# Kernel optimization log

Measured on AMD Instinct MI355X. Metric: run time of the kernel, lower is better.

The kernel has to match this reference:

```python
import jax, jax.numpy as jnp
import numpy as np

N_QUBITS = 11
N_CIRCUITS = 3
N_ROTS = 6
BATCH = 512
C64 = jnp.complex64


def _ry_mat(theta):
    # RY(t) = [[cos t/2, -sin t/2], [sin t/2, cos t/2]]
    c = jnp.cos(theta * 0.5)
    s = jnp.sin(theta * 0.5)
    return jnp.stack([jnp.stack([c, -s]), jnp.stack([s, c])]).astype(C64)


def _rz_mat(theta):
    # RZ(t) = diag(e^{-i t/2}, e^{+i t/2})
    e = jnp.exp((-0.5j) * theta.astype(C64))
    z = jnp.zeros_like(e)
    return jnp.stack([jnp.stack([e, z]), jnp.stack([z, jnp.conj(e)])])


def _apply_1q(state, U, q):
    # state: (2,)*n complex; apply 2x2 U on axis q (PennyLane wire q = axis q)
    out = jnp.tensordot(U, state, axes=((1,), (q,)))
    return jnp.moveaxis(out, 0, q)


def _apply_ctrl(state, U, c, t):
    # controlled-U on wires [c(control), t(target)]: block_diag(I2, U) in |c t> basis
    U4 = jnp.eye(4, dtype=C64).at[2:, 2:].set(U)
    out = jnp.tensordot(U4.reshape(2, 2, 2, 2), state, axes=((2, 3), (c, t)))
    return jnp.moveaxis(out, (0, 1), (c, t))


def _simulate(angles):
    # angles: [n_circuits, 6, n_qubits] -> expvals [2*n_qubits] (X then Z)
    n = N_QUBITS
    state = jnp.zeros((2,) * n, dtype=C64).at[(0,) * n].set(1.0)
    for i in range(N_CIRCUITS):
        for q in range(n):
            state = _apply_1q(state, _ry_mat(angles[i, 0, q]), q)
            state = _apply_1q(state, _rz_mat(angles[i, 1, q]), q)
            state = _apply_1q(state, _ry_mat(angles[i, 2, q]), q)
            state = _apply_1q(state, _rz_mat(angles[i, 3, q]), q)
        for q in range(n):
            t = (q + 1) % n
            state = _apply_ctrl(state, _ry_mat(angles[i, 4, q]), q, t)
            state = _apply_ctrl(state, _rz_mat(angles[i, 5, q]), q, t)
    ex_x, ex_z = [], []
    for q in range(n):
        s0 = jnp.take(state, 0, axis=q)
        s1 = jnp.take(state, 1, axis=q)
        # <X_q> = 2 Re <psi_{q=0}|psi_{q=1}>,  <Z_q> = p(q=0) - p(q=1)
        ex_x.append(2.0 * jnp.real(jnp.vdot(s0, s1)))
        ex_z.append(jnp.sum(jnp.abs(s0) ** 2 - jnp.abs(s1) ** 2))
    return jnp.stack(ex_x + ex_z).astype(jnp.float32)


def setup_inputs() -> dict:
    key = jax.random.key(0)
    k1, k2, k3 = jax.random.split(key, 3)
    x = jax.random.normal(k1, (BATCH, N_QUBITS), dtype=jnp.float32)
    W = jax.random.uniform(k2, (N_CIRCUITS, N_QUBITS * N_ROTS, N_QUBITS),
                           dtype=jnp.float32, minval=-0.01, maxval=0.01)
    b = jax.random.uniform(k3, (N_CIRCUITS, N_QUBITS * N_ROTS),
                           dtype=jnp.float32, minval=-0.01, maxval=0.01)
    return {"x": x, "W": W, "b": b}


def reference(x, W, b):
    # per-circuit Linear (dropout is identity in eval): [B, C, n_rots*n_qubits]
    rot = jnp.einsum('coi,bi->bco', W, x) + b[None, :, :]
    angles = rot.reshape(x.shape[0], N_CIRCUITS, N_ROTS, N_QUBITS)
    return jax.vmap(_simulate)(angles)  # [B, 2*n_qubits]
```

## Files before the change

### kernel.cpp

```cpp
#include <hip/hip_runtime.h>

#define NQ 11
#define NC 3
#define NANG (NC * 66)
#define BLOCK 512

typedef float f2 __attribute__((ext_vector_type(2)));

__device__ __forceinline__ f2 swp(f2 v) { return __builtin_shufflevector(v, v, 1, 0); }

template<int CTRL>
__device__ __forceinline__ float dppx(float v) {
  return __int_as_float(__builtin_amdgcn_update_dpp(
      0, __float_as_int(v), CTRL, 0xF, 0xF, false));
}
template<int CTRL>
__device__ __forceinline__ f2 dpp2(f2 v) {
  f2 r; r.x = dppx<CTRL>(v.x); r.y = dppx<CTRL>(v.y); return r;
}
template<int OFF>
__device__ __forceinline__ float swz1(float v) {
  return __int_as_float(__builtin_amdgcn_ds_swizzle(__float_as_int(v), OFF));
}
template<int OFF>
__device__ __forceinline__ f2 swz2(f2 v) {
  f2 r; r.x = swz1<OFF>(v.x); r.y = swz1<OFF>(v.y); return r;
}
__device__ __forceinline__ float plp16(float v, int lane) {
  auto r = __builtin_amdgcn_permlane16_swap(__float_as_int(v), __float_as_int(v), false, false);
  return __int_as_float((lane & 16) ? r[0] : r[1]);
}
__device__ __forceinline__ float plp32(float v, int lane) {
  auto r = __builtin_amdgcn_permlane32_swap(__float_as_int(v), __float_as_int(v), false, false);
  return __int_as_float((lane & 32) ? r[0] : r[1]);
}
__device__ __forceinline__ f2 plp16_2(f2 v, int lane) {
  f2 r; r.x = plp16(v.x, lane); r.y = plp16(v.y, lane); return r;
}
__device__ __forceinline__ f2 plp32_2(f2 v, int lane) {
  f2 r; r.x = plp32(v.x, lane); r.y = plp32(v.y, lane); return r;
}
__device__ __forceinline__ float plsum16(float v) {
  auto r = __builtin_amdgcn_permlane16_swap(__float_as_int(v), __float_as_int(v), false, false);
  return __int_as_float(r[0]) + __int_as_float(r[1]);
}
__device__ __forceinline__ float plsum32(float v) {
  auto r = __builtin_amdgcn_permlane32_swap(__float_as_int(v), __float_as_int(v), false, false);
  return __int_as_float(r[0]) + __int_as_float(r[1]);
}

__device__ __forceinline__ void apply2p(f2& v0, f2& v1, float4 U) {
  const f2 ai2 = {-U.y, U.y};
  const f2 bi2 = {-U.w, U.w};
  const f2 w0 = swp(v0), w1 = swp(v1);
  const f2 n0 =  U.x * v0 + ai2 * w0 + U.z * v1 + bi2 * w1;
  const f2 n1 = -U.z * v0 + bi2 * w0 + U.x * v1 - ai2 * w1;
  v0 = n0; v1 = n1;
}
__device__ __forceinline__ void gpartp(f2& v, f2 p, float4 U, bool hi) {
  const f2 ai2 = hi ? f2{U.y, -U.y} : f2{-U.y, U.y};
  const float br = hi ? -U.z : U.z;
  const f2 bi2 = {-U.w, U.w};
  v = U.x * v + ai2 * swp(v) + br * p + bi2 * swp(p);
}

__device__ __forceinline__ f2 cmul(f2 u, f2 v) {
  return f2{u.x * v.x - u.y * v.y, u.x * v.y + u.y * v.x};
}
__device__ __forceinline__ void rowof(float4 G, bool hi, f2& c0, f2& c1) {
  c0 = hi ? f2{-G.z, G.w} : f2{G.x, G.y};
  c1 = hi ? f2{G.x, -G.y} : f2{G.z, G.w};
}

__device__ __forceinline__ void g_wave3(f2 (&s)[4], float4 A, float4 B, float4 C,
                                        f2* __restrict__ buf, int wave, int lane) {
  const int base = (wave << 6) | lane;
#pragma unroll
  for (int i = 0; i < 4; ++i) buf[(i << 9) | base] = s[i];
  f2 a0, a1, b0, b1, c0, c1;
  rowof(A, (wave & 4) != 0, a0, a1);
  rowof(B, (wave & 2) != 0, b0, b1);
  rowof(C, (wave & 1) != 0, c0, c1);
  const f2 d00 = cmul(b0, c0), d01 = cmul(b0, c1);
  const f2 d10 = cmul(b1, c0), d11 = cmul(b1, c1);
  f2 r[8];
  r[0] = cmul(a0, d00); r[1] = cmul(a0, d01); r[2] = cmul(a0, d10); r[3] = cmul(a0, d11);
  r[4] = cmul(a1, d00); r[5] = cmul(a1, d01); r[6] = cmul(a1, d10); r[7] = cmul(a1, d11);
  __syncthreads();
#pragma unroll
  for (int i = 0; i < 4; ++i) {
    f2 acc = {0.f, 0.f};
#pragma unroll
    for (int w2 = 0; w2 < 8; ++w2) {
      const f2 p = buf[(i << 9) | (w2 << 6) | lane];
      acc += r[w2].x * p + f2{-r[w2].y, r[w2].y} * swp(p);
    }
    s[i] = acc;
  }
}

__global__ __launch_bounds__(BLOCK) void qsim_kernel(
    const float* __restrict__ x, const float* __restrict__ W,
    const float* __restrict__ bias, float* __restrict__ out) {
  const int bidx = blockIdx.x;
  const int tid = threadIdx.x;
  const int lane = tid & 63, wave = tid >> 6;

  __shared__ float xs[NQ];
  __shared__ float ang[NANG];
  __shared__ float4 m1s[NC * NQ];
  __shared__ float4 m2s[NC * NQ];
  __shared__ float4 v1s[NC * 10];
  __shared__ f2 ex0[2048];
  __shared__ f2 ex1[2048];
  __shared__ float red[8][24];

  if (tid < NQ) xs[tid] = x[bidx * NQ + tid];
  __syncthreads();

  if (tid < NANG) {
    const int c = tid / 66, o = tid - c * 66;
    const float* wr = W + (c * 66 + o) * NQ;
    float s = bias[c * 66 + o];
#pragma unroll
    for (int i = 0; i < NQ; ++i) s += wr[i] * xs[i];
    ang[tid] = s;
  }
  __syncthreads();

  if (tid < 2 * NC * NQ) {
    const int kind = tid / (NC * NQ);
    const int id = tid - kind * (NC * NQ);
    const int c = id / NQ, q = id - c * NQ;
    const float* a = ang + c * 66;
    if (kind == 0) {
      float s0,c0,s1,c1,s2,c2,s3,c3;
      sincosf(0.5f*a[q],      &s0,&c0);
      sincosf(0.5f*a[11+q],   &s1,&c1);
      sincosf(0.5f*a[22+q],   &s2,&c2);
      sincosf(0.5f*a[33+q],   &s3,&c3);
      const float mar = c1*c0, mai = -s1*c0;
      const float mbr = -c1*s0, mbi = s1*s0;
      const float nar = c2*mar + s2*mbr, nai = c2*mai - s2*mbi;
      const float nbr = c2*mbr - s2*mar, nbi = c2*mbi + s2*mai;
      m1s[id] = make_float4(c3*nar + s3*nai, c3*nai - s3*nar,
                            c3*nbr + s3*nbi, c3*nbi - s3*nbr);
    } else {
      float s4,c4,s5,c5;
      sincosf(0.5f*a[44+q], &s4,&c4);
      sincosf(0.5f*a[55+q], &s5,&c5);
      m2s[id] = make_float4(c5*c4, -s5*c4, -c5*s4, s5*s4);
    }
  }
  __syncthreads();

  if (tid < NC * 10) {
    const int c = tid / 10, tt = tid - c * 10, t = tt + 1;
    const float4 A = m2s[c*NQ + t - 1];
    const float4 B = m1s[c*NQ + t];
    const float pr_=A.x, pi_=A.y, qr_=A.z, qi_=A.w;
    const float ar_=B.x, ai_=B.y, br_=B.z, bi_=B.w;
    v1s[c*10 + tt] = make_float4(
      (pr_*ar_ - pi_*ai_) - (qr_*br_ + qi_*bi_),
      (pr_*ai_ + pi_*ar_) - (qi_*br_ - qr_*bi_),
      (pr_*br_ - pi_*bi_) + (qr_*ar_ + qi_*ai_),
      (pr_*bi_ + pi_*br_) + (qi_*ar_ - qr_*ai_));
  }
  __syncthreads();

  f2 s[4];
#pragma unroll
  for (int i = 0; i < 4; ++i) s[i] = f2{0.f, 0.f};
  if (tid == 0) s[0].x = 1.f;

  for (int c = 0; c < NC; ++c) {
    const float4* M1 = &m1s[c * NQ];
    const float4* VF = &v1s[c * 10];
    {
      apply2p(s[0], s[1], M1[0]);
      apply2p(s[2], s[3], M1[0]);
    }
    g_pl32_regsel: ;
    {
      const bool hi = (lane & 32) != 0;
#pragma unroll
      for (int i = 0; i < 4; ++i)
        gpartp(s[i], plp32_2(s[i], lane), (i & 1) ? VF[0] : M1[1], hi);
    }
    {
      const float4 U = *((lane & 32) ? &VF[1] : &M1[2]);
      const bool hi = (lane & 16) != 0;
#pragma unroll
      for (int i = 0; i < 4; ++i) gpartp(s[i], plp16_2(s[i], lane), U, hi);
    }
    {
      const float4 U = *((lane & 16) ? &VF[2] : &M1[3]);
      const bool hi = (lane & 8) != 0;
#pragma unroll
      for (int i = 0; i < 4; ++i) gpartp(s[i], swz2<0x201F>(s[i]), U, hi);
    }
    {
      const float4 A = *((lane & 8) ? &VF[3] : &M1[4]);
      const float4 B = *((wave & 4) ? &VF[4] : &M1[5]);
      const float4 C = *((wave & 2) ? &VF[5] : &M1[6]);
      g_wave3(s, A, B, C, (c & 1) ? ex1 : ex0, wave, lane);
    }
    {
      const float4 U = *((wave & 1) ? &VF[6] : &M1[7]);
      const bool hi = (lane & 4) != 0;
#pragma unroll
      for (int i = 0; i < 4; ++i) gpartp(s[i], swz2<0x101F>(s[i]), U, hi);
    }
    {
      const float4 U = *((lane & 4) ? &VF[7] : &M1[8]);
      const bool hi = (lane & 2) != 0;
#pragma unroll
      for (int i = 0; i < 4; ++i) gpartp(s[i], dpp2<0x4E>(s[i]), U, hi);
    }
    {
      const float4 U = *((lane & 2) ? &VF[8] : &M1[9]);
      const bool hi = (lane & 1) != 0;
#pragma unroll
      for (int i = 0; i < 4; ++i) gpartp(s[i], dpp2<0xB1>(s[i]), U, hi);
    }
    {
      const float4 U = *((lane & 1) ? &VF[9] : &M1[10]);
      apply2p(s[0], s[2], U);
      apply2p(s[1], s[3], U);
    }
    {
      apply2p(s[2], s[3], m2s[c * NQ + 10]);
    }
  }

  f2* eb = ex1;
  const int base = (wave << 6) | lane;
#pragma unroll
  for (int i = 0; i < 4; ++i) eb[(i << 9) | base] = s[i];
  __syncthreads();
  const int pb4 = ((wave ^ 4) << 6) | lane;
  const int pb2 = ((wave ^ 2) << 6) | lane;
  const int pb1 = ((wave ^ 1) << 6) | lane;
  f2 aq4 = {0,0}, aq5 = {0,0}, aq6 = {0,0};
#pragma unroll
  for (int i = 0; i < 4; ++i) {
    aq4 += s[i] * eb[(i << 9) | pb4];
    aq5 += s[i] * eb[(i << 9) | pb2];
    aq6 += s[i] * eb[(i << 9) | pb1];
  }
  f2 mg[4];
#pragma unroll
  for (int i = 0; i < 4; ++i) mg[i] = s[i] * s[i];
  const f2 ztv  = (mg[0] + mg[1]) + (mg[2] + mg[3]);
  const f2 z0v  = (mg[0] - mg[1]) + (mg[2] - mg[3]);
  const f2 z10v = (mg[0] + mg[1]) - (mg[2] + mg[3]);
  f2 aq0={0,0}, aq10={0,0}, aq9={0,0}, aq8={0,0}, aq7={0,0}, aq3={0,0}, aq2={0,0}, aq1={0,0};
#pragma unroll
  for (int i = 0; i < 4; ++i) {
    aq0  += s[i] * s[i ^ 1];
    aq10 += s[i] * s[i ^ 2];
    aq9  += s[i] * dpp2<0xB1>(s[i]);
    aq8  += s[i] * dpp2<0x4E>(s[i]);
    aq7  += s[i] * swz2<0x101F>(s[i]);
    aq3  += s[i] * swz2<0x201F>(s[i]);
    aq2  += s[i] * plp16_2(s[i], lane);
    aq1  += s[i] * plp32_2(s[i], lane);
  }
  const float ztot = ztv.x + ztv.y;

  float v[22];
  v[0]=aq0.x+aq0.y; v[1]=aq1.x+aq1.y; v[2]=aq2.x+aq2.y; v[3]=aq3.x+aq3.y;
  v[4]=aq4.x+aq4.y; v[5]=aq5.x+aq5.y; v[6]=aq6.x+aq6.y;
  v[7]=aq7.x+aq7.y; v[8]=aq8.x+aq8.y; v[9]=aq9.x+aq9.y; v[10]=aq10.x+aq10.y;
  v[11] = z0v.x + z0v.y;
  v[12] = (lane & 32) ? -ztot : ztot;
  v[13] = (lane & 16) ? -ztot : ztot;
  v[14] = (lane & 8)  ? -ztot : ztot;
  v[15] = (wave & 4)  ? -ztot : ztot;
  v[16] = (wave & 2)  ? -ztot : ztot;
  v[17] = (wave & 1)  ? -ztot : ztot;
  v[18] = (lane & 4)  ? -ztot : ztot;
  v[19] = (lane & 2)  ? -ztot : ztot;
  v[20] = (lane & 1)  ? -ztot : ztot;
  v[21] = z10v.x + z10v.y;

#pragma unroll
  for (int k = 0; k < 22; ++k) {
    v[k] += dppx<0xB1>(v[k]);
    v[k] += dppx<0x4E>(v[k]);
  }
  const int q4l = lane & 3;
  float wv[6];
#pragma unroll
  for (int p = 0; p < 5; ++p)
    wv[p] = q4l == 0 ? v[4*p] : (q4l == 1 ? v[4*p+1] : (q4l == 2 ? v[4*p+2] : v[4*p+3]));
  wv[5] = q4l == 0 ? v[20] : (q4l == 1 ? v[21] : 0.f);
#pragma unroll
  for (int p = 0; p < 6; ++p) {
    wv[p] += swz1<0x101F>(wv[p]);
    wv[p] += swz1<0x201F>(wv[p]);
    wv[p] = plsum16(wv[p]);
    wv[p] = plsum32(wv[p]);
  }
  if (lane < 4) {
#pragma unroll
    for (int p = 0; p < 6; ++p) red[wave][4*p + lane] = wv[p];
  }
  __syncthreads();
  if (tid < 22) {
    float sacc = 0.f;
#pragma unroll
    for (int w8 = 0; w8 < 8; ++w8) sacc += red[w8][tid];
    out[bidx * 22 + tid] = sacc;
  }
}

extern "C" void kernel_launch(void* const* d_in, const int* in_sizes, int n_in,
                              void* d_out, int out_size, void* d_ws, size_t ws_size,
                              hipStream_t stream) {
  (void)n_in; (void)d_ws; (void)ws_size; (void)out_size;
  const float* x = (const float*)d_in[0];
  const float* W = (const float*)d_in[1];
  const float* b = (const float*)d_in[2];
  float* out = (float*)d_out;
  const int batch = in_sizes[0] / NQ;
  qsim_kernel<<<batch, BLOCK, 0, stream>>>(x, W, b, out);
}
```

Baseline: 23.76 us.

## Compute gate matrices per wave and split cross-wave gate into pairwise exchanges

Each wave now redundantly computes the angles, rotation matrices and fused gate products in its own shared-memory slice. This removes the block-wide barriers from the setup phase. The three-qubit cross-wave gate is replaced by three pairwise exchanges through double-buffered shared memory, each reading one partner value instead of eight. The last controlled gate of each layer is also fused with the next layer's first single-qubit gate. In exchange, the cross-wave step needs three barriers per layer instead of one, and every wave repeats the setup work, including loads of W.

New measurement: 24.52 us. +3.2%, slower.

```diff
diff --git a/kernel.cpp b/kernel.cpp
--- a/kernel.cpp
+++ b/kernel.cpp
@@ -2,7 +2,6 @@
 
 #define NQ 11
 #define NC 3
-#define NANG (NC * 66)
 #define BLOCK 512
 
 typedef float f2 __attribute__((ext_vector_type(2)));
@@ -63,40 +62,23 @@
   const f2 bi2 = {-U.w, U.w};
   v = U.x * v + ai2 * swp(v) + br * p + bi2 * swp(p);
 }
-
-__device__ __forceinline__ f2 cmul(f2 u, f2 v) {
-  return f2{u.x * v.x - u.y * v.y, u.x * v.y + u.y * v.x};
-}
-__device__ __forceinline__ void rowof(float4 G, bool hi, f2& c0, f2& c1) {
-  c0 = hi ? f2{-G.z, G.w} : f2{G.x, G.y};
-  c1 = hi ? f2{G.x, -G.y} : f2{G.z, G.w};
-}
-
-__device__ __forceinline__ void g_wave3(f2 (&s)[4], float4 A, float4 B, float4 C,
-                                        f2* __restrict__ buf, int wave, int lane) {
+__device__ __forceinline__ float4 su2mul(float4 A, float4 B) {
+  return make_float4(
+    (A.x*B.x - A.y*B.y) - (A.z*B.z + A.w*B.w),
+    (A.x*B.y + A.y*B.x) - (A.w*B.z - A.z*B.w),
+    (A.x*B.z - A.y*B.w) + (A.z*B.x + A.w*B.y),
+    (A.x*B.w + A.y*B.z) + (A.w*B.x - A.z*B.y));
+}
+template<int WVX>
+__device__ __forceinline__ void g_wave(f2 (&s)[4], float4 U, f2* buf, int wave, int lane) {
   const int base = (wave << 6) | lane;
 #pragma unroll
   for (int i = 0; i < 4; ++i) buf[(i << 9) | base] = s[i];
-  f2 a0, a1, b0, b1, c0, c1;
-  rowof(A, (wave & 4) != 0, a0, a1);
-  rowof(B, (wave & 2) != 0, b0, b1);
-  rowof(C, (wave & 1) != 0, c0, c1);
-  const f2 d00 = cmul(b0, c0), d01 = cmul(b0, c1);
-  const f2 d10 = cmul(b1, c0), d11 = cmul(b1, c1);
-  f2 r[8];
-  r[0] = cmul(a0, d00); r[1] = cmul(a0, d01); r[2] = cmul(a0, d10); r[3] = cmul(a0, d11);
-  r[4] = cmul(a1, d00); r[5] = cmul(a1, d01); r[6] = cmul(a1, d10); r[7] = cmul(a1, d11);
   __syncthreads();
-#pragma unroll
-  for (int i = 0; i < 4; ++i) {
-    f2 acc = {0.f, 0.f};
-#pragma unroll
-    for (int w2 = 0; w2 < 8; ++w2) {
-      const f2 p = buf[(i << 9) | (w2 << 6) | lane];
-      acc += r[w2].x * p + f2{-r[w2].y, r[w2].y} * swp(p);
-    }
-    s[i] = acc;
-  }
+  const int pbase = ((wave ^ WVX) << 6) | lane;
+  const bool hi = (wave & WVX) != 0;
+#pragma unroll
+  for (int i = 0; i < 4; ++i) gpartp(s[i], buf[(i << 9) | pbase], U, hi);
 }
 
 __global__ __launch_bounds__(BLOCK) void qsim_kernel(
@@ -106,81 +88,95 @@
   const int tid = threadIdx.x;
   const int lane = tid & 63, wave = tid >> 6;
 
-  __shared__ float xs[NQ];
-  __shared__ float ang[NANG];
-  __shared__ float4 m1s[NC * NQ];
-  __shared__ float4 m2s[NC * NQ];
-  __shared__ float4 v1s[NC * 10];
+  __shared__ float  angw[8 * 198];
+  __shared__ float4 m1w[8 * 33];
+  __shared__ float4 m2w[8 * 33];
+  __shared__ float4 vw[8 * 30];
+  __shared__ float4 jw[8 * 2];
   __shared__ f2 ex0[2048];
   __shared__ f2 ex1[2048];
   __shared__ float red[8][24];
 
-  if (tid < NQ) xs[tid] = x[bidx * NQ + tid];
-  __syncthreads();
-
-  if (tid < NANG) {
-    const int c = tid / 66, o = tid - c * 66;
-    const float* wr = W + (c * 66 + o) * NQ;
-    float s = bias[c * 66 + o];
-#pragma unroll
-    for (int i = 0; i < NQ; ++i) s += wr[i] * xs[i];
-    ang[tid] = s;
-  }
-  __syncthreads();
-
-  if (tid < 2 * NC * NQ) {
-    const int kind = tid / (NC * NQ);
-    const int id = tid - kind * (NC * NQ);
+  float xr[NQ];
+#pragma unroll
+  for (int i = 0; i < NQ; ++i) xr[i] = x[bidx * NQ + i];
+
+  float* aw = angw + wave * 198;
+#pragma unroll
+  for (int r3 = 0; r3 < 3; ++r3) {
+    const int id = lane + 64 * r3;
+    const float* wr = W + id * NQ;
+    float s = bias[id];
+#pragma unroll
+    for (int i = 0; i < NQ; ++i) s += wr[i] * xr[i];
+    aw[id] = s;
+  }
+  if (lane < 6) {
+    const int id = 192 + lane;
+    const float* wr = W + id * NQ;
+    float s = bias[id];
+#pragma unroll
+    for (int i = 0; i < NQ; ++i) s += wr[i] * xr[i];
+    aw[id] = s;
+  }
+
+  float4* M1W = m1w + wave * 33;
+  float4* M2W = m2w + wave * 33;
+  float4* VW  = vw + wave * 30;
+  float4* JW  = jw + wave * 2;
+  if (lane < 33) {
+    const int id = lane, c = id / NQ, q = id - c * NQ;
+    const float* a = aw + c * 66;
+    float s0,c0,s1,c1,s2,c2,s3,c3;
+    sincosf(0.5f*a[q],      &s0,&c0);
+    sincosf(0.5f*a[11+q],   &s1,&c1);
+    sincosf(0.5f*a[22+q],   &s2,&c2);
+    sincosf(0.5f*a[33+q],   &s3,&c3);
+    const float mar = c1*c0, mai = -s1*c0;
+    const float mbr = -c1*s0, mbi = s1*s0;
+    const float nar = c2*mar + s2*mbr, nai = c2*mai - s2*mbi;
+    const float nbr = c2*mbr - s2*mar, nbi = c2*mbi + s2*mai;
+    M1W[id] = make_float4(c3*nar + s3*nai, c3*nai - s3*nar,
+                          c3*nbr + s3*nbi, c3*nbi - s3*nbr);
+  } else {
+    const int id = lane - 33;
     const int c = id / NQ, q = id - c * NQ;
-    const float* a = ang + c * 66;
-    if (kind == 0) {
-      float s0,c0,s1,c1,s2,c2,s3,c3;
-      sincosf(0.5f*a[q],      &s0,&c0);
-      sincosf(0.5f*a[11+q],   &s1,&c1);
-      sincosf(0.5f*a[22+q],   &s2,&c2);
-      sincosf(0.5f*a[33+q],   &s3,&c3);
-      const float mar = c1*c0, mai = -s1*c0;
-      const float mbr = -c1*s0, mbi = s1*s0;
-      const float nar = c2*mar + s2*mbr, nai = c2*mai - s2*mbi;
-      const float nbr = c2*mbr - s2*mar, nbi = c2*mbi + s2*mai;
-      m1s[id] = make_float4(c3*nar + s3*nai, c3*nai - s3*nar,
-                            c3*nbr + s3*nbi, c3*nbi - s3*nbr);
-    } else {
-      float s4,c4,s5,c5;
-      sincosf(0.5f*a[44+q], &s4,&c4);
-      sincosf(0.5f*a[55+q], &s5,&c5);
-      m2s[id] = make_float4(c5*c4, -s5*c4, -c5*s4, s5*s4);
-    }
-  }
-  __syncthreads();
-
-  if (tid < NC * 10) {
-    const int c = tid / 10, tt = tid - c * 10, t = tt + 1;
-    const float4 A = m2s[c*NQ + t - 1];
-    const float4 B = m1s[c*NQ + t];
-    const float pr_=A.x, pi_=A.y, qr_=A.z, qi_=A.w;
-    const float ar_=B.x, ai_=B.y, br_=B.z, bi_=B.w;
-    v1s[c*10 + tt] = make_float4(
-      (pr_*ar_ - pi_*ai_) - (qr_*br_ + qi_*bi_),
-      (pr_*ai_ + pi_*ar_) - (qi_*br_ - qr_*bi_),
-      (pr_*br_ - pi_*bi_) + (qr_*ar_ + qi_*ai_),
-      (pr_*bi_ + pi_*br_) + (qi_*ar_ - qr_*ai_));
-  }
-  __syncthreads();
+    const float* a = aw + c * 66;
+    float s4,c4,s5,c5;
+    sincosf(0.5f*a[44+q], &s4,&c4);
+    sincosf(0.5f*a[55+q], &s5,&c5);
+    M2W[id] = make_float4(c5*c4, -s5*c4, -c5*s4, s5*s4);
+  }
+  if (lane < 2) {
+    const int id = 31 + lane;
+    const int c = id / NQ, q = id - c * NQ;
+    const float* a = aw + c * 66;
+    float s4,c4,s5,c5;
+    sincosf(0.5f*a[44+q], &s4,&c4);
+    sincosf(0.5f*a[55+q], &s5,&c5);
+    M2W[id] = make_float4(c5*c4, -s5*c4, -c5*s4, s5*s4);
+  }
+  if (lane < 30) {
+    const int c = lane / 10, tt = lane - c * 10, t = tt + 1;
+    VW[lane] = su2mul(M2W[c*NQ + t - 1], M1W[c*NQ + t]);
+  } else if (lane < 32) {
+    const int cc = lane - 30;
+    JW[cc] = su2mul(M1W[(cc + 1) * NQ], M2W[cc * NQ + 10]);
+  }
 
   f2 s[4];
 #pragma unroll
   for (int i = 0; i < 4; ++i) s[i] = f2{0.f, 0.f};
   if (tid == 0) s[0].x = 1.f;
 
+  int par = 0;
   for (int c = 0; c < NC; ++c) {
-    const float4* M1 = &m1s[c * NQ];
-    const float4* VF = &v1s[c * 10];
-    {
+    const float4* M1 = M1W + c * NQ;
+    const float4* VF = VW + c * 10;
+    if (c == 0) {
       apply2p(s[0], s[1], M1[0]);
       apply2p(s[2], s[3], M1[0]);
     }
-    g_pl32_regsel: ;
     {
       const bool hi = (lane & 32) != 0;
 #pragma unroll
@@ -199,12 +195,9 @@
 #pragma unroll
       for (int i = 0; i < 4; ++i) gpartp(s[i], swz2<0x201F>(s[i]), U, hi);
     }
-    {
-      const float4 A = *((lane & 8) ? &VF[3] : &M1[4]);
-      const float4 B = *((wave & 4) ? &VF[4] : &M1[5]);
-      const float4 C = *((wave & 2) ? &VF[5] : &M1[6]);
-      g_wave3(s, A, B, C, (c & 1) ? ex1 : ex0, wave, lane);
-    }
+    g_wave<4>(s, *((lane & 8) ? &VF[3] : &M1[4]), par ? ex1 : ex0, wave, lane); par ^= 1;
+    g_wave<2>(s, *((wave & 4) ? &VF[4] : &M1[5]), par ? ex1 : ex0, wave, lane); par ^= 1;
+    g_wave<1>(s, *((wave & 2) ? &VF[5] : &M1[6]), par ? ex1 : ex0, wave, lane); par ^= 1;
     {
       const float4 U = *((wave & 1) ? &VF[6] : &M1[7]);
       const bool hi = (lane & 4) != 0;
@@ -228,12 +221,15 @@
       apply2p(s[0], s[2], U);
       apply2p(s[1], s[3], U);
     }
-    {
-      apply2p(s[2], s[3], m2s[c * NQ + 10]);
-    }
-  }
-
-  f2* eb = ex1;
+    if (c < 2) {
+      apply2p(s[0], s[1], M1W[(c + 1) * NQ]);
+      apply2p(s[2], s[3], JW[c]);
+    } else {
+      apply2p(s[2], s[3], M2W[32]);
+    }
+  }
+
+  f2* eb = par ? ex1 : ex0;
   const int base = (wave << 6) | lane;
 #pragma unroll
   for (int i = 0; i < 4; ++i) eb[(i << 9) | base] = s[i];
```

## Remap state to 256 threads with 8 amplitudes each, pairwise cross-wave gates

Applied to the files above, without the earlier changes.

Halves the block to 256 threads, so each thread holds 8 amplitudes instead of 4 and the 2048-amplitude state is remapped across lanes, waves and registers. The single three-qubit cross-wave gate through LDS is replaced by two one-qubit exchanges through LDS. The first gate of the next circuit is fused with the last controlled gate of the current one via precomputed SU(2) products. The aim is less LDS traffic per exchange and fewer threads per circuit, at the cost of more registers per thread, an extra barrier per circuit, and a rewired expectation-value mapping.

New measurement: 20.26 us (median of 2 runs). -14.7%, faster.

```diff
diff --git a/kernel.cpp b/kernel.cpp
--- a/kernel.cpp
+++ b/kernel.cpp
@@ -3,7 +3,7 @@
 #define NQ 11
 #define NC 3
 #define NANG (NC * 66)
-#define BLOCK 512
+#define BLOCK 256
 
 typedef float f2 __attribute__((ext_vector_type(2)));
 
@@ -63,40 +63,23 @@
   const f2 bi2 = {-U.w, U.w};
   v = U.x * v + ai2 * swp(v) + br * p + bi2 * swp(p);
 }
-
-__device__ __forceinline__ f2 cmul(f2 u, f2 v) {
-  return f2{u.x * v.x - u.y * v.y, u.x * v.y + u.y * v.x};
-}
-__device__ __forceinline__ void rowof(float4 G, bool hi, f2& c0, f2& c1) {
-  c0 = hi ? f2{-G.z, G.w} : f2{G.x, G.y};
-  c1 = hi ? f2{G.x, -G.y} : f2{G.z, G.w};
-}
-
-__device__ __forceinline__ void g_wave3(f2 (&s)[4], float4 A, float4 B, float4 C,
-                                        f2* __restrict__ buf, int wave, int lane) {
+__device__ __forceinline__ float4 su2mul(float4 A, float4 B) {
+  return make_float4(
+    (A.x*B.x - A.y*B.y) - (A.z*B.z + A.w*B.w),
+    (A.x*B.y + A.y*B.x) - (A.w*B.z - A.z*B.w),
+    (A.x*B.z - A.y*B.w) + (A.z*B.x + A.w*B.y),
+    (A.x*B.w + A.y*B.z) + (A.w*B.x - A.z*B.y));
+}
+template<int WVX>
+__device__ __forceinline__ void g_wave8(f2 (&s)[8], float4 U, f2* buf, int wave, int lane) {
   const int base = (wave << 6) | lane;
 #pragma unroll
-  for (int i = 0; i < 4; ++i) buf[(i << 9) | base] = s[i];
-  f2 a0, a1, b0, b1, c0, c1;
-  rowof(A, (wave & 4) != 0, a0, a1);
-  rowof(B, (wave & 2) != 0, b0, b1);
-  rowof(C, (wave & 1) != 0, c0, c1);
-  const f2 d00 = cmul(b0, c0), d01 = cmul(b0, c1);
-  const f2 d10 = cmul(b1, c0), d11 = cmul(b1, c1);
-  f2 r[8];
-  r[0] = cmul(a0, d00); r[1] = cmul(a0, d01); r[2] = cmul(a0, d10); r[3] = cmul(a0, d11);
-  r[4] = cmul(a1, d00); r[5] = cmul(a1, d01); r[6] = cmul(a1, d10); r[7] = cmul(a1, d11);
-  __syncthreads();
-#pragma unroll
-  for (int i = 0; i < 4; ++i) {
-    f2 acc = {0.f, 0.f};
-#pragma unroll
-    for (int w2 = 0; w2 < 8; ++w2) {
-      const f2 p = buf[(i << 9) | (w2 << 6) | lane];
-      acc += r[w2].x * p + f2{-r[w2].y, r[w2].y} * swp(p);
-    }
-    s[i] = acc;
-  }
+  for (int i = 0; i < 8; ++i) buf[(i << 8) | base] = s[i];
+  __syncthreads();
+  const int pbase = ((wave ^ WVX) << 6) | lane;
+  const bool hi = (wave & WVX) != 0;
+#pragma unroll
+  for (int i = 0; i < 8; ++i) gpartp(s[i], buf[(i << 8) | pbase], U, hi);
 }
 
 __global__ __launch_bounds__(BLOCK) void qsim_kernel(
@@ -111,9 +94,10 @@
   __shared__ float4 m1s[NC * NQ];
   __shared__ float4 m2s[NC * NQ];
   __shared__ float4 v1s[NC * 10];
+  __shared__ float4 js[2];
   __shared__ f2 ex0[2048];
   __shared__ f2 ex1[2048];
-  __shared__ float red[8][24];
+  __shared__ float red[4][24];
 
   if (tid < NQ) xs[tid] = x[bidx * NQ + tid];
   __syncthreads();
@@ -156,117 +140,124 @@
 
   if (tid < NC * 10) {
     const int c = tid / 10, tt = tid - c * 10, t = tt + 1;
-    const float4 A = m2s[c*NQ + t - 1];
-    const float4 B = m1s[c*NQ + t];
-    const float pr_=A.x, pi_=A.y, qr_=A.z, qi_=A.w;
-    const float ar_=B.x, ai_=B.y, br_=B.z, bi_=B.w;
-    v1s[c*10 + tt] = make_float4(
-      (pr_*ar_ - pi_*ai_) - (qr_*br_ + qi_*bi_),
-      (pr_*ai_ + pi_*ar_) - (qi_*br_ - qr_*bi_),
-      (pr_*br_ - pi_*bi_) + (qr_*ar_ + qi_*ai_),
-      (pr_*bi_ + pi_*br_) + (qi_*ar_ - qr_*ai_));
-  }
-  __syncthreads();
-
-  f2 s[4];
-#pragma unroll
-  for (int i = 0; i < 4; ++i) s[i] = f2{0.f, 0.f};
+    v1s[tid] = su2mul(m2s[c*NQ + t - 1], m1s[c*NQ + t]);
+  } else if (tid < NC * 10 + 2) {
+    const int cc = tid - NC * 10;
+    js[cc] = su2mul(m1s[(cc + 1) * NQ], m2s[cc * NQ + 10]);
+  }
+  __syncthreads();
+
+  f2 s[8];
+#pragma unroll
+  for (int i = 0; i < 8; ++i) s[i] = f2{0.f, 0.f};
   if (tid == 0) s[0].x = 1.f;
 
   for (int c = 0; c < NC; ++c) {
     const float4* M1 = &m1s[c * NQ];
     const float4* VF = &v1s[c * 10];
-    {
-      apply2p(s[0], s[1], M1[0]);
-      apply2p(s[2], s[3], M1[0]);
-    }
-    g_pl32_regsel: ;
+    if (c == 0) {
+      const float4 U = M1[0];
+#pragma unroll
+      for (int r = 0; r < 8; r += 2) apply2p(s[r], s[r + 1], U);
+    }
     {
       const bool hi = (lane & 32) != 0;
 #pragma unroll
-      for (int i = 0; i < 4; ++i)
-        gpartp(s[i], plp32_2(s[i], lane), (i & 1) ? VF[0] : M1[1], hi);
+      for (int r = 0; r < 8; ++r)
+        gpartp(s[r], plp32_2(s[r], lane), (r & 1) ? VF[0] : M1[1], hi);
     }
     {
       const float4 U = *((lane & 32) ? &VF[1] : &M1[2]);
       const bool hi = (lane & 16) != 0;
 #pragma unroll
-      for (int i = 0; i < 4; ++i) gpartp(s[i], plp16_2(s[i], lane), U, hi);
+      for (int r = 0; r < 8; ++r) gpartp(s[r], plp16_2(s[r], lane), U, hi);
     }
     {
       const float4 U = *((lane & 16) ? &VF[2] : &M1[3]);
       const bool hi = (lane & 8) != 0;
 #pragma unroll
-      for (int i = 0; i < 4; ++i) gpartp(s[i], swz2<0x201F>(s[i]), U, hi);
-    }
-    {
-      const float4 A = *((lane & 8) ? &VF[3] : &M1[4]);
-      const float4 B = *((wave & 4) ? &VF[4] : &M1[5]);
-      const float4 C = *((wave & 2) ? &VF[5] : &M1[6]);
-      g_wave3(s, A, B, C, (c & 1) ? ex1 : ex0, wave, lane);
-    }
+      for (int r = 0; r < 8; ++r) gpartp(s[r], swz2<0x201F>(s[r]), U, hi);
+    }
+    {
+      const float4 U = *((lane & 8) ? &VF[3] : &M1[4]);
+      const bool hi = (lane & 4) != 0;
+#pragma unroll
+      for (int r = 0; r < 8; ++r) gpartp(s[r], swz2<0x101F>(s[r]), U, hi);
+    }
+    g_wave8<2>(s, *((lane & 4) ? &VF[4] : &M1[5]), ex0, wave, lane);
+    g_wave8<1>(s, *((wave & 2) ? &VF[5] : &M1[6]), ex1, wave, lane);
     {
       const float4 U = *((wave & 1) ? &VF[6] : &M1[7]);
-      const bool hi = (lane & 4) != 0;
-#pragma unroll
-      for (int i = 0; i < 4; ++i) gpartp(s[i], swz2<0x101F>(s[i]), U, hi);
-    }
-    {
-      const float4 U = *((lane & 4) ? &VF[7] : &M1[8]);
       const bool hi = (lane & 2) != 0;
 #pragma unroll
-      for (int i = 0; i < 4; ++i) gpartp(s[i], dpp2<0x4E>(s[i]), U, hi);
-    }
-    {
-      const float4 U = *((lane & 2) ? &VF[8] : &M1[9]);
+      for (int r = 0; r < 8; ++r) gpartp(s[r], dpp2<0x4E>(s[r]), U, hi);
+    }
+    {
+      const float4 U = *((lane & 2) ? &VF[7] : &M1[8]);
       const bool hi = (lane & 1) != 0;
 #pragma unroll
-      for (int i = 0; i < 4; ++i) gpartp(s[i], dpp2<0xB1>(s[i]), U, hi);
-    }
-    {
-      const float4 U = *((lane & 1) ? &VF[9] : &M1[10]);
-      apply2p(s[0], s[2], U);
-      apply2p(s[1], s[3], U);
-    }
-    {
-      apply2p(s[2], s[3], m2s[c * NQ + 10]);
-    }
-  }
-
-  f2* eb = ex1;
+      for (int r = 0; r < 8; ++r) gpartp(s[r], dpp2<0xB1>(s[r]), U, hi);
+    }
+    {
+      const float4 U = *((lane & 1) ? &VF[8] : &M1[9]);
+      apply2p(s[0], s[2], U); apply2p(s[1], s[3], U);
+      apply2p(s[4], s[6], U); apply2p(s[5], s[7], U);
+    }
+    {
+      const float4 U0 = M1[10], U1 = VF[9];
+      apply2p(s[0], s[4], U0); apply2p(s[1], s[5], U0);
+      apply2p(s[2], s[6], U1); apply2p(s[3], s[7], U1);
+    }
+    if (c < 2) {
+      const float4 Un = m1s[(c + 1) * NQ];
+      const float4 Uj = js[c];
+      apply2p(s[0], s[1], Un); apply2p(s[2], s[3], Un);
+      apply2p(s[4], s[5], Uj); apply2p(s[6], s[7], Uj);
+    } else {
+      const float4 U = m2s[c * NQ + 10];
+      apply2p(s[4], s[5], U); apply2p(s[6], s[7], U);
+    }
+  }
+
   const int base = (wave << 6) | lane;
 #pragma unroll
-  for (int i = 0; i < 4; ++i) eb[(i << 9) | base] = s[i];
-  __syncthreads();
-  const int pb4 = ((wave ^ 4) << 6) | lane;
+  for (int i = 0; i < 8; ++i) ex0[(i << 8) | base] = s[i];
+  __syncthreads();
   const int pb2 = ((wave ^ 2) << 6) | lane;
   const int pb1 = ((wave ^ 1) << 6) | lane;
-  f2 aq4 = {0,0}, aq5 = {0,0}, aq6 = {0,0};
-#pragma unroll
-  for (int i = 0; i < 4; ++i) {
-    aq4 += s[i] * eb[(i << 9) | pb4];
-    aq5 += s[i] * eb[(i << 9) | pb2];
-    aq6 += s[i] * eb[(i << 9) | pb1];
-  }
-  f2 mg[4];
-#pragma unroll
-  for (int i = 0; i < 4; ++i) mg[i] = s[i] * s[i];
-  const f2 ztv  = (mg[0] + mg[1]) + (mg[2] + mg[3]);
-  const f2 z0v  = (mg[0] - mg[1]) + (mg[2] - mg[3]);
-  const f2 z10v = (mg[0] + mg[1]) - (mg[2] + mg[3]);
-  f2 aq0={0,0}, aq10={0,0}, aq9={0,0}, aq8={0,0}, aq7={0,0}, aq3={0,0}, aq2={0,0}, aq1={0,0};
-#pragma unroll
-  for (int i = 0; i < 4; ++i) {
-    aq0  += s[i] * s[i ^ 1];
-    aq10 += s[i] * s[i ^ 2];
-    aq9  += s[i] * dpp2<0xB1>(s[i]);
-    aq8  += s[i] * dpp2<0x4E>(s[i]);
-    aq7  += s[i] * swz2<0x101F>(s[i]);
-    aq3  += s[i] * swz2<0x201F>(s[i]);
-    aq2  += s[i] * plp16_2(s[i], lane);
-    aq1  += s[i] * plp32_2(s[i], lane);
-  }
-  const float ztot = ztv.x + ztv.y;
+  f2 aq5 = {0,0}, aq6 = {0,0};
+#pragma unroll
+  for (int i = 0; i < 8; ++i) {
+    aq5 += s[i] * ex0[(i << 8) | pb2];
+    aq6 += s[i] * ex0[(i << 8) | pb1];
+  }
+  f2 zt = {0,0}, z0v = {0,0}, z9v = {0,0}, z10v = {0,0};
+#pragma unroll
+  for (int r = 0; r < 8; ++r) {
+    const f2 m = s[r] * s[r];
+    zt += m;
+    z0v  += (r & 1) ? -m : m;
+    z9v  += (r & 2) ? -m : m;
+    z10v += (r & 4) ? -m : m;
+  }
+  f2 aq0 = {0,0}, aq9 = {0,0}, aq10 = {0,0};
+#pragma unroll
+  for (int r = 0; r < 8; ++r) {
+    aq0  += s[r] * s[r ^ 1];
+    aq9  += s[r] * s[r ^ 2];
+    aq10 += s[r] * s[r ^ 4];
+  }
+  f2 aq1={0,0}, aq2={0,0}, aq3={0,0}, aq4={0,0}, aq7={0,0}, aq8={0,0};
+#pragma unroll
+  for (int r = 0; r < 8; ++r) {
+    aq1 += s[r] * plp32_2(s[r], lane);
+    aq2 += s[r] * plp16_2(s[r], lane);
+    aq3 += s[r] * swz2<0x201F>(s[r]);
+    aq4 += s[r] * swz2<0x101F>(s[r]);
+    aq7 += s[r] * dpp2<0x4E>(s[r]);
+    aq8 += s[r] * dpp2<0xB1>(s[r]);
+  }
+  const float ztot = zt.x + zt.y;
 
   float v[22];
   v[0]=aq0.x+aq0.y; v[1]=aq1.x+aq1.y; v[2]=aq2.x+aq2.y; v[3]=aq3.x+aq3.y;
@@ -276,12 +267,12 @@
   v[12] = (lane & 32) ? -ztot : ztot;
   v[13] = (lane & 16) ? -ztot : ztot;
   v[14] = (lane & 8)  ? -ztot : ztot;
-  v[15] = (wave & 4)  ? -ztot : ztot;
+  v[15] = (lane & 4)  ? -ztot : ztot;
   v[16] = (wave & 2)  ? -ztot : ztot;
   v[17] = (wave & 1)  ? -ztot : ztot;
-  v[18] = (lane & 4)  ? -ztot : ztot;
-  v[19] = (lane & 2)  ? -ztot : ztot;
-  v[20] = (lane & 1)  ? -ztot : ztot;
+  v[18] = (lane & 2)  ? -ztot : ztot;
+  v[19] = (lane & 1)  ? -ztot : ztot;
+  v[20] = z9v.x + z9v.y;
   v[21] = z10v.x + z10v.y;
 
 #pragma unroll
@@ -310,7 +301,7 @@
   if (tid < 22) {
     float sacc = 0.f;
 #pragma unroll
-    for (int w8 = 0; w8 < 8; ++w8) sacc += red[w8][tid];
+    for (int w4 = 0; w4 < 4; ++w4) sacc += red[w4][tid];
     out[bidx * 22 + tid] = sacc;
   }
 }
```
